# Kernel optimization log

Measured on AMD Instinct MI355X. Metric: run time of the kernel, lower is better.

## Reference

```python
import jax, jax.numpy as jnp
import numpy as np

N = 50000      # nodes
E = 800000     # edges (avg degree 16)
D = 128        # in_channels
H = 128        # hidden_channels


def sage_conv(x, edge_index, W_l, b_l, W_r):
    """PyG SAGEConv with aggr='mean': lin_l(mean_j x_j) + lin_r(x_i).
    edge_index[0] = source (j), edge_index[1] = destination (i)."""
    src, dst = edge_index[0], edge_index[1]
    n = x.shape[0]
    msg = x[src]                                               # [E, D] gather
    agg = jax.ops.segment_sum(msg, dst, num_segments=n)        # [N, D] scatter-sum
    cnt = jax.ops.segment_sum(jnp.ones((src.shape[0],), x.dtype), dst, num_segments=n)
    agg = agg / jnp.maximum(cnt, 1.0)[:, None]                 # mean (0 for isolated nodes)
    return agg @ W_l.T + b_l + x @ W_r.T


def setup_inputs() -> dict:
    key = jax.random.key(0)
    ks = jax.random.split(key, 9)
    s_in = 1.0 / np.sqrt(D)
    s_h = 1.0 / np.sqrt(H)
    return {
        "x": jax.random.normal(ks[0], (N, D), dtype=jnp.float32),
        "edge_index": jax.random.randint(ks[1], (2, E), 0, N, dtype=jnp.int64),
        "W1l": jax.random.uniform(ks[2], (H, D), jnp.float32, -s_in, s_in),
        "b1l": jnp.zeros((H,), jnp.float32),
        "W1r": jax.random.uniform(ks[3], (H, D), jnp.float32, -s_in, s_in),
        "W2l": jax.random.uniform(ks[4], (H, H), jnp.float32, -s_h, s_h),
        "b2l": jnp.zeros((H,), jnp.float32),
        "W2r": jax.random.uniform(ks[5], (H, H), jnp.float32, -s_h, s_h),
        "W3l": jax.random.uniform(ks[6], (H, H), jnp.float32, -s_h, s_h),
        "b3l": jnp.zeros((H,), jnp.float32),
        "W3r": jax.random.uniform(ks[7], (H, H), jnp.float32, -s_h, s_h),
    }


def reference(x, edge_index, W1l, b1l, W1r, W2l, b2l, W2r, W3l, b3l, W3r):
    x1 = sage_conv(x, edge_index, W1l, b1l, W1r)
    x1 = jax.nn.relu(x1)  # Dropout(0.5) treated as identity (eval mode)
    h_ = sage_conv(x1, edge_index, W2l, b2l, W2r)
    h = sage_conv(x1, edge_index, W3l, b3l, W3r)
    return (h_, h)
```

## Files before the change

kernel.cpp:

```cpp
#include <hip/hip_runtime.h>
#include <stdint.h>
#include <math.h>

typedef __attribute__((ext_vector_type(8))) short short8;
typedef __attribute__((ext_vector_type(4))) float float4v;

__device__ __forceinline__ uint16_t f2bf(float f){
  union { float f; uint32_t i; } c; c.f = f;
  uint32_t r = c.i + 0x7fffu + ((c.i >> 16) & 1u);
  return (uint16_t)(r >> 16);
}
__device__ __forceinline__ uint32_t pack2(float lo, float hi){
  return (uint32_t)f2bf(lo) | ((uint32_t)f2bf(hi) << 16);
}
__device__ __forceinline__ void acc_bf2(uint32_t w, float& x, float& y){
  union { uint32_t i; float f; } a, b;
  a.i = w << 16; b.i = w & 0xffff0000u;
  x += a.f; y += b.f;
}
__device__ __forceinline__ void accum8(uint4 v, float* a){
  acc_bf2(v.x, a[0], a[1]); acc_bf2(v.y, a[2], a[3]);
  acc_bf2(v.z, a[4], a[5]); acc_bf2(v.w, a[6], a[7]);
}


__global__ __launch_bounds__(512) void prep_kernel(
    const int* __restrict__ ei, int E, int NB, int CAP, int p1blk,
    int* __restrict__ fill, uint32_t* __restrict__ bins,
    const float* __restrict__ x,
    const float* __restrict__ w0, const float* __restrict__ w1,
    const float* __restrict__ w2, const float* __restrict__ w3,
    const float* __restrict__ w4, const float* __restrict__ w5,
    uint16_t* __restrict__ xb, uint16_t* __restrict__ wb, int nx){
  if ((int)blockIdx.x < p1blk){
    __shared__ int hist[256], scn[256], cursor[256], gbase[256], excl[256];
    __shared__ uint32_t stage[4096];
    int tid = threadIdx.x;
    if (tid < 256) hist[tid] = 0;
    __syncthreads();
    int e0 = blockIdx.x * 4096;
    int nval = E - e0; if (nval > 4096) nval = 4096;
    uint32_t w[8]; int bk[8];
    #pragma unroll
    for (int k = 0; k < 8; ++k){
      int e = e0 + k * 512 + tid;
      bool ok = e < E;
      int s = ok ? ei[e] : 0;
      int d = ok ? ei[E + e] : 0;
      w[k] = (uint32_t)s | ((uint32_t)d << 16);
      bk[k] = ok ? (d >> 8) : -1;
      if (ok) atomicAdd(&hist[bk[k]], 1);
    }
    __syncthreads();
    if (tid < 256) scn[tid] = hist[tid];
    __syncthreads();
    #pragma unroll
    for (int off = 1; off < 256; off <<= 1){
      int v = 0;
      if (tid < 256 && tid >= off) v = scn[tid - off];
      __syncthreads();
      if (tid < 256) scn[tid] += v;
      __syncthreads();
    }
    if (tid < 256){
      int ex = scn[tid] - hist[tid];
      excl[tid] = ex; cursor[tid] = ex;
      gbase[tid] = (tid < NB && hist[tid] > 0)
                   ? atomicAdd(&fill[tid], hist[tid]) : 0;
    }
    __syncthreads();
    #pragma unroll
    for (int k = 0; k < 8; ++k){
      if (bk[k] >= 0){
        int p = atomicAdd(&cursor[bk[k]], 1);
        stage[p] = w[k];
      }
    }
    __syncthreads();
    for (int i = tid; i < nval; i += 512){
      uint32_t v = stage[i];
      int b = v >> 24;
      int loc = gbase[b] + (i - excl[b]);
      if (loc < CAP)
        __builtin_nontemporal_store(v, bins + (size_t)b * CAP + loc);
    }
  } else {
    int i = (blockIdx.x - p1blk) * 512 + threadIdx.x;
    int stride = (gridDim.x - p1blk) * 512;
    for (int j = i; j < (nx >> 2); j += stride){
      float4 v = ((const float4*)x)[j];
      uint2 o;
      o.x = pack2(v.x, v.y); o.y = pack2(v.z, v.w);
      ((uint2*)xb)[j] = o;
    }
    const int WSZ = 128 * 128;
    for (int j = i; j < 6 * WSZ; j += stride){
      int t = j >> 14, o = j & (WSZ - 1);
      const float* w = t == 0 ? w0 : t == 1 ? w1 : t == 2 ? w2 : t == 3 ? w3 : t == 4 ? w4 : w5;
      wb[j] = f2bf(w[o]);
    }
  }
}


__global__ __launch_bounds__(512) void build_kernel(const uint32_t* __restrict__ bins,
                                                    const int* __restrict__ fill,
                                                    int CAP, int n,
                                                    int2* __restrict__ rowptr2,
                                                    uint32_t* __restrict__ esrc){
  __shared__ int hist[256], scn[256], cursor[256], excl[256];
  __shared__ uint32_t stage[5120];
  int b = blockIdx.x, tid = threadIdx.x;
  int cnt = fill[b]; if (cnt > CAP) cnt = CAP; if (cnt > 5120) cnt = 5120;
  size_t gb = (size_t)b * CAP;
  if (tid < 256) hist[tid] = 0;
  __syncthreads();
  for (int i = tid; i < cnt; i += 512)
    atomicAdd(&hist[(bins[gb + i] >> 16) & 255], 1);
  __syncthreads();
  if (tid < 256) scn[tid] = hist[tid];
  __syncthreads();
  #pragma unroll
  for (int off = 1; off < 256; off <<= 1){
    int v = 0;
    if (tid < 256 && tid >= off) v = scn[tid - off];
    __syncthreads();
    if (tid < 256) scn[tid] += v;
    __syncthreads();
  }
  if (tid < 256){
    int ex = scn[tid] - hist[tid];
    excl[tid] = ex; cursor[tid] = ex;
    int node = (b << 8) + tid;
    if (node < n) rowptr2[node] = make_int2((int)gb + ex, (int)gb + scn[tid]);
  }
  __syncthreads();
  for (int i = tid; i < cnt; i += 512){
    uint32_t v = bins[gb + i];
    int p = atomicAdd(&cursor[(v >> 16) & 255], 1);
    stage[p] = v & 0xffffu;
  }
  __syncthreads();
  for (int i = tid; i < cnt; i += 512)
    __builtin_nontemporal_store(stage[i], esrc + gb + i);
}


__global__ __launch_bounds__(256) void agg_kernel(const uint16_t* __restrict__ xin,
                                                  const int2* __restrict__ rowptr2,
                                                  const uint32_t* __restrict__ esrc,
                                                  uint16_t* __restrict__ aggw, int n){
  int node = blockIdx.x * 4 + (threadIdx.x >> 6);
  if (node >= n) return;
  int lane = threadIdx.x & 63;
  int sub = lane >> 4, fq = lane & 15;
  const uint4* xv = (const uint4*)xin;
  int2 be = rowptr2[node];
  int beg = be.x, end = be.y;
  float inv = 1.f / fmaxf((float)(end - beg), 1.f);
  float a[8] = {0.f,0.f,0.f,0.f,0.f,0.f,0.f,0.f};
  int e = beg + sub;
  for (; e + 12 < end; e += 16){
    int s0 = esrc[e], s1 = esrc[e + 4], s2 = esrc[e + 8], s3 = esrc[e + 12];
    uint4 v0 = xv[(size_t)s0 * 16 + fq];
    uint4 v1 = xv[(size_t)s1 * 16 + fq];
    uint4 v2 = xv[(size_t)s2 * 16 + fq];
    uint4 v3 = xv[(size_t)s3 * 16 + fq];
    accum8(v0, a); accum8(v1, a); accum8(v2, a); accum8(v3, a);
  }
  for (; e < end; e += 4){
    uint4 v = xv[(size_t)esrc[e] * 16 + fq];
    accum8(v, a);
  }
  #pragma unroll
  for (int i = 0; i < 8; ++i){
    a[i] += __shfl_xor(a[i], 16);
    a[i] += __shfl_xor(a[i], 32);
    a[i] *= inv;
  }
  if (sub == 0){
    uint4 o;
    o.x = pack2(a[0], a[1]); o.y = pack2(a[2], a[3]);
    o.z = pack2(a[4], a[5]); o.w = pack2(a[6], a[7]);
    ((uint4*)aggw)[(size_t)node * 16 + fq] = o;
  }
}


#define WT_STRIDE 136

__device__ __forceinline__ void stage_weights(const uint16_t* __restrict__ Wl,
                                              const uint16_t* __restrict__ Wr,
                                              int ch, uint16_t* lds_l,
                                              uint16_t* lds_r, int tid){
  const uint4* srcL = (const uint4*)(Wl + (size_t)(ch * 64) * 128);
  const uint4* srcR = (const uint4*)(Wr + (size_t)(ch * 64) * 128);
  #pragma unroll
  for (int i = 0; i < 4; ++i){
    int j = tid + i * 256;
    int row = j >> 4, c8 = j & 15;
    uint4 vl = srcL[j], vr = srcR[j];
    *(uint4*)(lds_l + row * WT_STRIDE + c8 * 8) = vl;
    *(uint4*)(lds_r + row * WT_STRIDE + c8 * 8) = vr;
  }
}

__global__ __launch_bounds__(256) void gemm1_kernel(
    const uint16_t* __restrict__ Aagg, const uint16_t* __restrict__ Ax,
    const uint16_t* __restrict__ Wl, const uint16_t* __restrict__ Wr,
    const float* __restrict__ bias, uint16_t* __restrict__ x1b, int n){
  __shared__ uint16_t lds_l[64 * WT_STRIDE], lds_r[64 * WT_STRIDE];
  int tid = threadIdx.x, lane = tid & 63, wid = tid >> 6;
  int m = lane & 15, quad = lane >> 4;
  int r0 = blockIdx.x * 64 + wid * 16;
  int arow = r0 + m; if (arow > n - 1) arow = n - 1;

  short8 a0f[4], a1f[4];
  #pragma unroll
  for (int ks = 0; ks < 4; ++ks){
    a0f[ks] = *(const short8*)(Aagg + (size_t)arow * 128 + ks * 32 + quad * 8);
    a1f[ks] = *(const short8*)(Ax   + (size_t)arow * 128 + ks * 32 + quad * 8);
  }

  for (int ch = 0; ch < 2; ++ch){
    if (ch) __syncthreads();
    stage_weights(Wl, Wr, ch, lds_l, lds_r, tid);
    __syncthreads();
    float4v acc[4];
    #pragma unroll
    for (int ct = 0; ct < 4; ++ct) acc[ct] = (float4v){0.f, 0.f, 0.f, 0.f};
    #pragma unroll
    for (int ks = 0; ks < 4; ++ks){
      #pragma unroll
      for (int ct = 0; ct < 4; ++ct){
        short8 b0 = *(const short8*)(lds_l + (ct * 16 + m) * WT_STRIDE + ks * 32 + quad * 8);
        acc[ct] = __builtin_amdgcn_mfma_f32_16x16x32_bf16(a0f[ks], b0, acc[ct], 0, 0, 0);
        short8 b1 = *(const short8*)(lds_r + (ct * 16 + m) * WT_STRIDE + ks * 32 + quad * 8);
        acc[ct] = __builtin_amdgcn_mfma_f32_16x16x32_bf16(a1f[ks], b1, acc[ct], 0, 0, 0);
      }
    }
    #pragma unroll
    for (int ct = 0; ct < 4; ++ct){
      int col = ch * 64 + ct * 16 + m;
      float bv = bias[col];
      #pragma unroll
      for (int i = 0; i < 4; ++i){
        int grow = r0 + quad * 4 + i;
        if (grow < n)
          x1b[(size_t)grow * 128 + col] = f2bf(fmaxf(acc[ct][i] + bv, 0.f));
      }
    }
  }
}

__global__ __launch_bounds__(256) void gemm23_kernel(
    const uint16_t* __restrict__ Aagg, const uint16_t* __restrict__ Ax,
    const uint16_t* __restrict__ W2l, const uint16_t* __restrict__ W2r,
    const float* __restrict__ b2,
    const uint16_t* __restrict__ W3l, const uint16_t* __restrict__ W3r,
    const float* __restrict__ b3,
    float* __restrict__ out, size_t half, int n){
  __shared__ uint16_t lds_l[64 * WT_STRIDE], lds_r[64 * WT_STRIDE];
  int tid = threadIdx.x, lane = tid & 63, wid = tid >> 6;
  int m = lane & 15, quad = lane >> 4;
  int r0 = blockIdx.x * 64 + wid * 16;
  int arow = r0 + m; if (arow > n - 1) arow = n - 1;

  short8 a0f[4], a1f[4];
  #pragma unroll
  for (int ks = 0; ks < 4; ++ks){
    a0f[ks] = *(const short8*)(Aagg + (size_t)arow * 128 + ks * 32 + quad * 8);
    a1f[ks] = *(const short8*)(Ax   + (size_t)arow * 128 + ks * 32 + quad * 8);
  }

  for (int idx = 0; idx < 4; ++idx){
    int pass = idx >> 1, ch = idx & 1;
    if (idx) __syncthreads();
    stage_weights(pass ? W3l : W2l, pass ? W3r : W2r, ch, lds_l, lds_r, tid);
    __syncthreads();
    float4v acc[4];
    #pragma unroll
    for (int ct = 0; ct < 4; ++ct) acc[ct] = (float4v){0.f, 0.f, 0.f, 0.f};
    #pragma unroll
    for (int ks = 0; ks < 4; ++ks){
      #pragma unroll
      for (int ct = 0; ct < 4; ++ct){
        short8 b0 = *(const short8*)(lds_l + (ct * 16 + m) * WT_STRIDE + ks * 32 + quad * 8);
        acc[ct] = __builtin_amdgcn_mfma_f32_16x16x32_bf16(a0f[ks], b0, acc[ct], 0, 0, 0);
        short8 b1 = *(const short8*)(lds_r + (ct * 16 + m) * WT_STRIDE + ks * 32 + quad * 8);
        acc[ct] = __builtin_amdgcn_mfma_f32_16x16x32_bf16(a1f[ks], b1, acc[ct], 0, 0, 0);
      }
    }
    const float* bb = pass ? b3 : b2;
    float* op = out + (pass ? half : 0);
    #pragma unroll
    for (int ct = 0; ct < 4; ++ct){
      int col = ch * 64 + ct * 16 + m;
      float bv = bb[col];
      #pragma unroll
      for (int i = 0; i < 4; ++i){
        int grow = r0 + quad * 4 + i;
        if (grow < n)
          __builtin_nontemporal_store(acc[ct][i] + bv,
                                      op + (size_t)grow * 128 + col);
      }
    }
  }
}


extern "C" void kernel_launch(void* const* d_in, const int* in_sizes, int n_in,
                              void* d_out, int out_size, void* d_ws, size_t ws_size,
                              hipStream_t stream) {
  const float* x   = (const float*)d_in[0];
  const int*   ei  = (const int*)d_in[1];
  const float* W1l = (const float*)d_in[2];
  const float* b1l = (const float*)d_in[3];
  const float* W1r = (const float*)d_in[4];
  const float* W2l = (const float*)d_in[5];
  const float* b2l = (const float*)d_in[6];
  const float* W2r = (const float*)d_in[7];
  const float* W3l = (const float*)d_in[8];
  const float* b3l = (const float*)d_in[9];
  const float* W3r = (const float*)d_in[10];
  float* out = (float*)d_out;

  const int n = in_sizes[0] / 128;
  const int E = in_sizes[1] / 2;
  const size_t half = (size_t)n * 128;
  const int WSZ = 128 * 128;

  const int NB = (n + 255) >> 8;
  int mean = (E + NB - 1) / NB;
  int CAP = mean + 8 * (int)sqrt((double)mean) + 64;
  CAP = (CAP + 63) & ~63;
  if (CAP > 5120) CAP = 5120;

  size_t off = 0;
  auto carve = [&](size_t bytes) -> void* {
    void* p = (char*)d_ws + off;
    off += (bytes + 255) & ~(size_t)255;
    return p;
  };
  int2*     rowptr2 = (int2*)carve((size_t)n * 8);
  int*      fill    = (int*)carve((size_t)NB * 4);
  uint32_t* esrc    = (uint32_t*)carve((size_t)NB * CAP * 4);
  uint16_t* xb      = (uint16_t*)carve(half * 2);
  uint16_t* wb      = (uint16_t*)carve((size_t)6 * WSZ * 2);
  uint16_t* x1b     = (uint16_t*)carve(half * 2);
  uint16_t* agg     = (uint16_t*)carve(half * 2);
  uint32_t* bins    = (uint32_t*)carve((size_t)NB * CAP * 4);
  (void)ws_size;

  hipMemsetAsync(fill, 0, (size_t)NB * 4, stream);

  int p1blk = (E + 4095) / 4096;
  int cblk  = 512;
  prep_kernel<<<p1blk + cblk, 512, 0, stream>>>(ei, E, NB, CAP, p1blk, fill, bins,
                                                x, W1l, W1r, W2l, W2r, W3l, W3r,
                                                xb, wb, (int)half);
  build_kernel<<<NB, 512, 0, stream>>>(bins, fill, CAP, n, rowptr2, esrc);

  int ablk = (n + 3) / 4;
  int gblk = (n + 63) / 64;
  const uint16_t *Wb1l = wb, *Wb1r = wb + WSZ, *Wb2l = wb + 2 * WSZ,
                 *Wb2r = wb + 3 * WSZ, *Wb3l = wb + 4 * WSZ, *Wb3r = wb + 5 * WSZ;

  agg_kernel<<<ablk, 256, 0, stream>>>(xb, rowptr2, esrc, agg, n);
  gemm1_kernel<<<gblk, 256, 0, stream>>>(agg, xb, Wb1l, Wb1r, b1l, x1b, n);

  agg_kernel<<<ablk, 256, 0, stream>>>(x1b, rowptr2, esrc, agg, n);
  gemm23_kernel<<<gblk, 256, 0, stream>>>(agg, x1b, Wb2l, Wb2r, b2l,
                                          Wb3l, Wb3r, b3l, out, half, n);
}
```

Baseline: 215.6 us.

## Split CSR build into quarter-bin blocks and parallelize gemm23 over passes

The edge binning pass now handles 2048 edges per block instead of 4096, and more blocks go to the conversion work. The CSR build kernel is split four ways per bin: each block redoes the bin histogram but only scatters the 64 nodes in its quarter, which raises parallelism and shrinks shared-memory staging. The layer-2/3 GEMM kernel gets a second grid dimension so each pass (W2 vs W3) runs in its own block. The cost is redundant histogram work and rereading each bin four times, plus the A fragments being loaded twice across the pass blocks.

```diff
diff --git a/kernel.cpp b/kernel.cpp
--- a/kernel.cpp
+++ b/kernel.cpp
@@ -23,6 +23,8 @@
   acc_bf2(v.z, a[4], a[5]); acc_bf2(v.w, a[6], a[7]);
 }
 
+
+#define P1_EPT 4
 
 __global__ __launch_bounds__(512) void prep_kernel(
     const int* __restrict__ ei, int E, int NB, int CAP, int p1blk,
@@ -34,15 +36,15 @@
     uint16_t* __restrict__ xb, uint16_t* __restrict__ wb, int nx){
   if ((int)blockIdx.x < p1blk){
     __shared__ int hist[256], scn[256], cursor[256], gbase[256], excl[256];
-    __shared__ uint32_t stage[4096];
+    __shared__ uint32_t stage[2048];
     int tid = threadIdx.x;
     if (tid < 256) hist[tid] = 0;
     __syncthreads();
-    int e0 = blockIdx.x * 4096;
-    int nval = E - e0; if (nval > 4096) nval = 4096;
-    uint32_t w[8]; int bk[8];
-    #pragma unroll
-    for (int k = 0; k < 8; ++k){
+    int e0 = blockIdx.x * 2048;
+    int nval = E - e0; if (nval > 2048) nval = 2048;
+    uint32_t w[P1_EPT]; int bk[P1_EPT];
+    #pragma unroll
+    for (int k = 0; k < P1_EPT; ++k){
       int e = e0 + k * 512 + tid;
       bool ok = e < E;
       int s = ok ? ei[e] : 0;
@@ -70,7 +72,7 @@
     }
     __syncthreads();
     #pragma unroll
-    for (int k = 0; k < 8; ++k){
+    for (int k = 0; k < P1_EPT; ++k){
       if (bk[k] >= 0){
         int p = atomicAdd(&cursor[bk[k]], 1);
         stage[p] = w[k];
@@ -108,10 +110,11 @@
                                                     int CAP, int n,
                                                     int2* __restrict__ rowptr2,
                                                     uint32_t* __restrict__ esrc){
-  __shared__ int hist[256], scn[256], cursor[256], excl[256];
-  __shared__ uint32_t stage[5120];
-  int b = blockIdx.x, tid = threadIdx.x;
-  int cnt = fill[b]; if (cnt > CAP) cnt = CAP; if (cnt > 5120) cnt = 5120;
+  __shared__ int hist[256], scn[256], cursor[64];
+  __shared__ uint32_t stage[4096];
+  int blk = blockIdx.x, tid = threadIdx.x;
+  int b = blk >> 2, q = blk & 3;
+  int cnt = fill[b]; if (cnt > CAP) cnt = CAP;
   size_t gb = (size_t)b * CAP;
   if (tid < 256) hist[tid] = 0;
   __syncthreads();
@@ -128,21 +131,30 @@
     if (tid < 256) scn[tid] += v;
     __syncthreads();
   }
-  if (tid < 256){
-    int ex = scn[tid] - hist[tid];
-    excl[tid] = ex; cursor[tid] = ex;
-    int node = (b << 8) + tid;
-    if (node < n) rowptr2[node] = make_int2((int)gb + ex, (int)gb + scn[tid]);
+  int q0 = q * 64;
+  int qstart = scn[q0] - hist[q0];
+  int qend = scn[q0 + 63];
+  if (tid < 64){
+    int idx = q0 + tid;
+    int node = (b << 8) + idx;
+    int ex = scn[idx] - hist[idx];
+    cursor[tid] = ex - qstart;
+    if (node < n) rowptr2[node] = make_int2((int)gb + ex, (int)gb + scn[idx]);
   }
   __syncthreads();
   for (int i = tid; i < cnt; i += 512){
     uint32_t v = bins[gb + i];
-    int p = atomicAdd(&cursor[(v >> 16) & 255], 1);
-    stage[p] = v & 0xffffu;
-  }
-  __syncthreads();
-  for (int i = tid; i < cnt; i += 512)
-    __builtin_nontemporal_store(stage[i], esrc + gb + i);
+    int nb = (v >> 16) & 255;
+    int r = nb - q0;
+    if ((unsigned)r < 64u){
+      int p = atomicAdd(&cursor[r], 1);
+      if (p < 4096) stage[p] = v & 0xffffu;
+    }
+  }
+  __syncthreads();
+  int qcnt = qend - qstart; if (qcnt > 4096) qcnt = 4096;
+  for (int i = tid; i < qcnt; i += 512)
+    __builtin_nontemporal_store(stage[i], esrc + gb + qstart + i);
 }
 
 
@@ -263,6 +275,11 @@
   __shared__ uint16_t lds_l[64 * WT_STRIDE], lds_r[64 * WT_STRIDE];
   int tid = threadIdx.x, lane = tid & 63, wid = tid >> 6;
   int m = lane & 15, quad = lane >> 4;
+  int pass = blockIdx.y;
+  const uint16_t* Wl = pass ? W3l : W2l;
+  const uint16_t* Wr = pass ? W3r : W2r;
+  const float*    bb = pass ? b3  : b2;
+  float* op = out + (pass ? half : 0);
   int r0 = blockIdx.x * 64 + wid * 16;
   int arow = r0 + m; if (arow > n - 1) arow = n - 1;
 
@@ -273,10 +290,9 @@
     a1f[ks] = *(const short8*)(Ax   + (size_t)arow * 128 + ks * 32 + quad * 8);
   }
 
-  for (int idx = 0; idx < 4; ++idx){
-    int pass = idx >> 1, ch = idx & 1;
-    if (idx) __syncthreads();
-    stage_weights(pass ? W3l : W2l, pass ? W3r : W2r, ch, lds_l, lds_r, tid);
+  for (int ch = 0; ch < 2; ++ch){
+    if (ch) __syncthreads();
+    stage_weights(Wl, Wr, ch, lds_l, lds_r, tid);
     __syncthreads();
     float4v acc[4];
     #pragma unroll
@@ -291,8 +307,6 @@
         acc[ct] = __builtin_amdgcn_mfma_f32_16x16x32_bf16(a1f[ks], b1, acc[ct], 0, 0, 0);
       }
     }
-    const float* bb = pass ? b3 : b2;
-    float* op = out + (pass ? half : 0);
     #pragma unroll
     for (int ct = 0; ct < 4; ++ct){
       int col = ch * 64 + ct * 16 + m;
@@ -354,12 +368,12 @@
 
   hipMemsetAsync(fill, 0, (size_t)NB * 4, stream);
 
-  int p1blk = (E + 4095) / 4096;
-  int cblk  = 512;
+  int p1blk = (E + 2047) / 2048;
+  int cblk  = 768;
   prep_kernel<<<p1blk + cblk, 512, 0, stream>>>(ei, E, NB, CAP, p1blk, fill, bins,
                                                 x, W1l, W1r, W2l, W2r, W3l, W3r,
                                                 xb, wb, (int)half);
-  build_kernel<<<NB, 512, 0, stream>>>(bins, fill, CAP, n, rowptr2, esrc);
+  build_kernel<<<NB * 4, 512, 0, stream>>>(bins, fill, CAP, n, rowptr2, esrc);
 
   int ablk = (n + 3) / 4;
   int gblk = (n + 63) / 64;
@@ -370,6 +384,6 @@
   gemm1_kernel<<<gblk, 256, 0, stream>>>(agg, xb, Wb1l, Wb1r, b1l, x1b, n);
 
   agg_kernel<<<ablk, 256, 0, stream>>>(x1b, rowptr2, esrc, agg, n);
-  gemm23_kernel<<<gblk, 256, 0, stream>>>(agg, x1b, Wb2l, Wb2r, b2l,
-                                          Wb3l, Wb3r, b3l, out, half, n);
-}
+  gemm23_kernel<<<dim3(gblk, 2), 256, 0, stream>>>(agg, x1b, Wb2l, Wb2r, b2l,
+                                                   Wb3l, Wb3r, b3l, out, half, n);
+}
```

New measurement: 222.6 us. 3.3% more time.

## Fuse all pipeline stages into one cooperative persistent kernel with grid syncs

Applied to the files above, without the earlier changes.

Replaces the six separate kernel launches (prep, build, two agg, two gemm) with a single cooperative mega-kernel that uses grid-wide syncs between phases and grid-stride loops over work. The aim is to remove launch overhead and inter-kernel gaps. In exchange, occupancy is bounded by the persistent grid size, and grid.sync barriers add cost. The old multi-kernel path is kept as a fallback if the cooperative launch fails. It also drops a 5120 clamp in build_kernel that guarded the stage buffer.

```diff
diff --git a/kernel.cpp b/kernel.cpp
--- a/kernel.cpp
+++ b/kernel.cpp
@@ -1,6 +1,9 @@
 #include <hip/hip_runtime.h>
+#include <hip/hip_cooperative_groups.h>
 #include <stdint.h>
 #include <math.h>
+
+namespace cg = cooperative_groups;
 
 typedef __attribute__((ext_vector_type(8))) short short8;
 typedef __attribute__((ext_vector_type(4))) float float4v;
@@ -21,6 +24,308 @@
 __device__ __forceinline__ void accum8(uint4 v, float* a){
   acc_bf2(v.x, a[0], a[1]); acc_bf2(v.y, a[2], a[3]);
   acc_bf2(v.z, a[4], a[5]); acc_bf2(v.w, a[6], a[7]);
+}
+
+#define WT_STRIDE 136
+
+
+struct MegaParams {
+  const int* ei;
+  const float *x, *W1l, *b1l, *W1r, *W2l, *b2l, *W2r, *W3l, *b3l, *W3r;
+  float* out;
+  int* fill; uint32_t* bins; uint32_t* esrc; int2* rowptr2;
+  uint16_t *xb, *wb, *x1b, *agg;
+  int E, n, NB, CAP, p1blk;
+  size_t half;
+};
+
+__device__ __forceinline__ void agg_phase(const uint16_t* __restrict__ xin,
+                                          const int2* __restrict__ rowptr2,
+                                          const uint32_t* __restrict__ esrc,
+                                          uint16_t* __restrict__ aggw,
+                                          int n, int tid, int bid, int gsz){
+  int wid = tid >> 6, lane = tid & 63;
+  int sub = lane >> 4, fq = lane & 15;
+  const uint4* xv = (const uint4*)xin;
+  for (int node = bid * 8 + wid; node < n; node += gsz * 8){
+    int2 be = rowptr2[node];
+    int beg = be.x, end = be.y;
+    float inv = 1.f / fmaxf((float)(end - beg), 1.f);
+    float a[8] = {0.f,0.f,0.f,0.f,0.f,0.f,0.f,0.f};
+    int e = beg + sub;
+    for (; e + 12 < end; e += 16){
+      int s0 = esrc[e], s1 = esrc[e + 4], s2 = esrc[e + 8], s3 = esrc[e + 12];
+      uint4 v0 = xv[(size_t)s0 * 16 + fq];
+      uint4 v1 = xv[(size_t)s1 * 16 + fq];
+      uint4 v2 = xv[(size_t)s2 * 16 + fq];
+      uint4 v3 = xv[(size_t)s3 * 16 + fq];
+      accum8(v0, a); accum8(v1, a); accum8(v2, a); accum8(v3, a);
+    }
+    for (; e < end; e += 4){
+      uint4 v = xv[(size_t)esrc[e] * 16 + fq];
+      accum8(v, a);
+    }
+    #pragma unroll
+    for (int i = 0; i < 8; ++i){
+      a[i] += __shfl_xor(a[i], 16);
+      a[i] += __shfl_xor(a[i], 32);
+      a[i] *= inv;
+    }
+    if (sub == 0){
+      uint4 o;
+      o.x = pack2(a[0], a[1]); o.y = pack2(a[2], a[3]);
+      o.z = pack2(a[4], a[5]); o.w = pack2(a[6], a[7]);
+      ((uint4*)aggw)[(size_t)node * 16 + fq] = o;
+    }
+  }
+}
+
+__device__ __forceinline__ void stage_weights512(const uint16_t* __restrict__ Wl,
+                                                 const uint16_t* __restrict__ Wr,
+                                                 int ch, uint16_t* lds_l,
+                                                 uint16_t* lds_r, int tid){
+  const uint4* srcL = (const uint4*)(Wl + (size_t)(ch * 64) * 128);
+  const uint4* srcR = (const uint4*)(Wr + (size_t)(ch * 64) * 128);
+  #pragma unroll
+  for (int i = 0; i < 2; ++i){
+    int j = tid + i * 512;
+    int row = j >> 4, c8 = j & 15;
+    uint4 vl = srcL[j], vr = srcR[j];
+    *(uint4*)(lds_l + row * WT_STRIDE + c8 * 8) = vl;
+    *(uint4*)(lds_r + row * WT_STRIDE + c8 * 8) = vr;
+  }
+}
+
+__global__ __launch_bounds__(512, 6) void mega_kernel(MegaParams P){
+  cg::grid_group gg = cg::this_grid();
+  __shared__ __align__(16) uint8_t smem[34816];
+  const int tid = threadIdx.x, bid = blockIdx.x, gsz = gridDim.x;
+  const int WSZ = 128 * 128;
+
+  if (bid < P.p1blk){
+    int* hist = (int*)smem;
+    int* scn  = hist + 256;
+    int* cur  = hist + 512;
+    int* gbas = hist + 768;
+    int* excl = hist + 1024;
+    uint32_t* stg = (uint32_t*)(smem + 5120);
+    if (tid < 256) hist[tid] = 0;
+    __syncthreads();
+    int e0 = bid * 4096;
+    int nval = P.E - e0; if (nval > 4096) nval = 4096;
+    uint32_t w[8]; int bk[8];
+    #pragma unroll
+    for (int k = 0; k < 8; ++k){
+      int e = e0 + k * 512 + tid;
+      bool ok = e < P.E;
+      int s = ok ? P.ei[e] : 0;
+      int d = ok ? P.ei[P.E + e] : 0;
+      w[k] = (uint32_t)s | ((uint32_t)d << 16);
+      bk[k] = ok ? (d >> 8) : -1;
+      if (ok) atomicAdd(&hist[bk[k]], 1);
+    }
+    __syncthreads();
+    if (tid < 256) scn[tid] = hist[tid];
+    __syncthreads();
+    #pragma unroll
+    for (int off = 1; off < 256; off <<= 1){
+      int v = 0;
+      if (tid < 256 && tid >= off) v = scn[tid - off];
+      __syncthreads();
+      if (tid < 256) scn[tid] += v;
+      __syncthreads();
+    }
+    if (tid < 256){
+      int ex = scn[tid] - hist[tid];
+      excl[tid] = ex; cur[tid] = ex;
+      gbas[tid] = (tid < P.NB && hist[tid] > 0)
+                  ? atomicAdd(&P.fill[tid], hist[tid]) : 0;
+    }
+    __syncthreads();
+    #pragma unroll
+    for (int k = 0; k < 8; ++k){
+      if (bk[k] >= 0){
+        int p = atomicAdd(&cur[bk[k]], 1);
+        stg[p] = w[k];
+      }
+    }
+    __syncthreads();
+    for (int i = tid; i < nval; i += 512){
+      uint32_t v = stg[i];
+      int b = v >> 24;
+      int loc = gbas[b] + (i - excl[b]);
+      if (loc < P.CAP)
+        __builtin_nontemporal_store(v, P.bins + (size_t)b * P.CAP + loc);
+    }
+  } else {
+    int i0 = (bid - P.p1blk) * 512 + tid;
+    int stride = (gsz - P.p1blk) * 512;
+    int nx4 = (P.n * 128) >> 2;
+    for (int j = i0; j < nx4; j += stride){
+      float4 v = ((const float4*)P.x)[j];
+      uint2 o; o.x = pack2(v.x, v.y); o.y = pack2(v.z, v.w);
+      ((uint2*)P.xb)[j] = o;
+    }
+    for (int j = i0; j < 6 * WSZ; j += stride){
+      int t = j >> 14, o = j & (WSZ - 1);
+      const float* w = t == 0 ? P.W1l : t == 1 ? P.W1r : t == 2 ? P.W2l
+                     : t == 3 ? P.W2r : t == 4 ? P.W3l : P.W3r;
+      P.wb[j] = f2bf(w[o]);
+    }
+  }
+  gg.sync();
+
+  for (int b = bid; b < P.NB; b += gsz){
+    int* hist = (int*)smem; int* scn = hist + 256; int* cursor = hist + 512;
+    uint32_t* stage = (uint32_t*)(smem + 3072);
+    int cnt = P.fill[b]; if (cnt > P.CAP) cnt = P.CAP;
+    size_t gb = (size_t)b * P.CAP;
+    if (tid < 256) hist[tid] = 0;
+    __syncthreads();
+    for (int i = tid; i < cnt; i += 512)
+      atomicAdd(&hist[(P.bins[gb + i] >> 16) & 255], 1);
+    __syncthreads();
+    if (tid < 256) scn[tid] = hist[tid];
+    __syncthreads();
+    #pragma unroll
+    for (int off = 1; off < 256; off <<= 1){
+      int v = 0;
+      if (tid < 256 && tid >= off) v = scn[tid - off];
+      __syncthreads();
+      if (tid < 256) scn[tid] += v;
+      __syncthreads();
+    }
+    if (tid < 256){
+      int ex = scn[tid] - hist[tid];
+      cursor[tid] = ex;
+      int node = (b << 8) + tid;
+      if (node < P.n) P.rowptr2[node] = make_int2((int)gb + ex, (int)gb + scn[tid]);
+    }
+    __syncthreads();
+    for (int i = tid; i < cnt; i += 512){
+      uint32_t v = P.bins[gb + i];
+      int p = atomicAdd(&cursor[(v >> 16) & 255], 1);
+      stage[p] = v & 0xffffu;
+    }
+    __syncthreads();
+    for (int i = tid; i < cnt; i += 512)
+      __builtin_nontemporal_store(stage[i], P.esrc + gb + i);
+    __syncthreads();
+  }
+  gg.sync();
+
+  agg_phase(P.xb, P.rowptr2, P.esrc, P.agg, P.n, tid, bid, gsz);
+  gg.sync();
+
+  {
+    uint16_t* lds_l = (uint16_t*)smem;
+    uint16_t* lds_r = lds_l + 64 * WT_STRIDE;
+    int lane = tid & 63, wid = tid >> 6;
+    int m = lane & 15, quad = lane >> 4;
+    const uint16_t* Wl = P.wb;
+    const uint16_t* Wr = P.wb + WSZ;
+    int ngt = (P.n + 63) >> 6;
+    int nt2 = (ngt + 1) >> 1;
+    for (int t2 = bid; t2 < nt2; t2 += gsz){
+      int tile = t2 * 2 + (wid >> 2);
+      int r0 = tile * 64 + (wid & 3) * 16;
+      int arow = r0 + m; if (arow > P.n - 1) arow = P.n - 1;
+      short8 a0f[4], a1f[4];
+      #pragma unroll
+      for (int ks = 0; ks < 4; ++ks){
+        a0f[ks] = *(const short8*)(P.agg + (size_t)arow * 128 + ks * 32 + quad * 8);
+        a1f[ks] = *(const short8*)(P.xb  + (size_t)arow * 128 + ks * 32 + quad * 8);
+      }
+      for (int ch = 0; ch < 2; ++ch){
+        __syncthreads();
+        stage_weights512(Wl, Wr, ch, lds_l, lds_r, tid);
+        __syncthreads();
+        float4v acc[4];
+        #pragma unroll
+        for (int ct = 0; ct < 4; ++ct) acc[ct] = (float4v){0.f, 0.f, 0.f, 0.f};
+        #pragma unroll
+        for (int ks = 0; ks < 4; ++ks){
+          #pragma unroll
+          for (int ct = 0; ct < 4; ++ct){
+            short8 b0 = *(const short8*)(lds_l + (ct * 16 + m) * WT_STRIDE + ks * 32 + quad * 8);
+            acc[ct] = __builtin_amdgcn_mfma_f32_16x16x32_bf16(a0f[ks], b0, acc[ct], 0, 0, 0);
+            short8 b1 = *(const short8*)(lds_r + (ct * 16 + m) * WT_STRIDE + ks * 32 + quad * 8);
+            acc[ct] = __builtin_amdgcn_mfma_f32_16x16x32_bf16(a1f[ks], b1, acc[ct], 0, 0, 0);
+          }
+        }
+        #pragma unroll
+        for (int ct = 0; ct < 4; ++ct){
+          int col = ch * 64 + ct * 16 + m;
+          float bv = P.b1l[col];
+          #pragma unroll
+          for (int i = 0; i < 4; ++i){
+            int grow = r0 + quad * 4 + i;
+            if (grow < P.n)
+              P.x1b[(size_t)grow * 128 + col] = f2bf(fmaxf(acc[ct][i] + bv, 0.f));
+          }
+        }
+      }
+    }
+  }
+  gg.sync();
+
+  agg_phase(P.x1b, P.rowptr2, P.esrc, P.agg, P.n, tid, bid, gsz);
+  gg.sync();
+
+  {
+    uint16_t* lds_l = (uint16_t*)smem;
+    uint16_t* lds_r = lds_l + 64 * WT_STRIDE;
+    int lane = tid & 63, wid = tid >> 6;
+    int m = lane & 15, quad = lane >> 4;
+    int ngt = (P.n + 63) >> 6;
+    int nt2 = (ngt + 1) >> 1;
+    for (int t2 = bid; t2 < nt2; t2 += gsz){
+      int tile = t2 * 2 + (wid >> 2);
+      int r0 = tile * 64 + (wid & 3) * 16;
+      int arow = r0 + m; if (arow > P.n - 1) arow = P.n - 1;
+      short8 a0f[4], a1f[4];
+      #pragma unroll
+      for (int ks = 0; ks < 4; ++ks){
+        a0f[ks] = *(const short8*)(P.agg + (size_t)arow * 128 + ks * 32 + quad * 8);
+        a1f[ks] = *(const short8*)(P.x1b + (size_t)arow * 128 + ks * 32 + quad * 8);
+      }
+      for (int idx = 0; idx < 4; ++idx){
+        int pass = idx >> 1, ch = idx & 1;
+        const uint16_t* Wl = P.wb + (pass ? 4 : 2) * WSZ;
+        const uint16_t* Wr = P.wb + (pass ? 5 : 3) * WSZ;
+        __syncthreads();
+        stage_weights512(Wl, Wr, ch, lds_l, lds_r, tid);
+        __syncthreads();
+        float4v acc[4];
+        #pragma unroll
+        for (int ct = 0; ct < 4; ++ct) acc[ct] = (float4v){0.f, 0.f, 0.f, 0.f};
+        #pragma unroll
+        for (int ks = 0; ks < 4; ++ks){
+          #pragma unroll
+          for (int ct = 0; ct < 4; ++ct){
+            short8 b0 = *(const short8*)(lds_l + (ct * 16 + m) * WT_STRIDE + ks * 32 + quad * 8);
+            acc[ct] = __builtin_amdgcn_mfma_f32_16x16x32_bf16(a0f[ks], b0, acc[ct], 0, 0, 0);
+            short8 b1 = *(const short8*)(lds_r + (ct * 16 + m) * WT_STRIDE + ks * 32 + quad * 8);
+            acc[ct] = __builtin_amdgcn_mfma_f32_16x16x32_bf16(a1f[ks], b1, acc[ct], 0, 0, 0);
+          }
+        }
+        const float* bb = pass ? P.b3l : P.b2l;
+        float* op = P.out + (pass ? P.half : 0);
+        #pragma unroll
+        for (int ct = 0; ct < 4; ++ct){
+          int col = ch * 64 + ct * 16 + m;
+          float bv = bb[col];
+          #pragma unroll
+          for (int i = 0; i < 4; ++i){
+            int grow = r0 + quad * 4 + i;
+            if (grow < P.n)
+              __builtin_nontemporal_store(acc[ct][i] + bv,
+                                          op + (size_t)grow * 128 + col);
+          }
+        }
+      }
+    }
+  }
 }
 
 
@@ -102,16 +407,15 @@
   }
 }
 
-
 __global__ __launch_bounds__(512) void build_kernel(const uint32_t* __restrict__ bins,
                                                     const int* __restrict__ fill,
                                                     int CAP, int n,
                                                     int2* __restrict__ rowptr2,
                                                     uint32_t* __restrict__ esrc){
-  __shared__ int hist[256], scn[256], cursor[256], excl[256];
+  __shared__ int hist[256], scn[256], cursor[256];
   __shared__ uint32_t stage[5120];
   int b = blockIdx.x, tid = threadIdx.x;
-  int cnt = fill[b]; if (cnt > CAP) cnt = CAP; if (cnt > 5120) cnt = 5120;
+  int cnt = fill[b]; if (cnt > CAP) cnt = CAP;
   size_t gb = (size_t)b * CAP;
   if (tid < 256) hist[tid] = 0;
   __syncthreads();
@@ -130,7 +434,7 @@
   }
   if (tid < 256){
     int ex = scn[tid] - hist[tid];
-    excl[tid] = ex; cursor[tid] = ex;
+    cursor[tid] = ex;
     int node = (b << 8) + tid;
     if (node < n) rowptr2[node] = make_int2((int)gb + ex, (int)gb + scn[tid]);
   }
@@ -144,7 +448,6 @@
   for (int i = tid; i < cnt; i += 512)
     __builtin_nontemporal_store(stage[i], esrc + gb + i);
 }
-
 
 __global__ __launch_bounds__(256) void agg_kernel(const uint16_t* __restrict__ xin,
                                                   const int2* __restrict__ rowptr2,
@@ -186,9 +489,6 @@
   }
 }
 
-
-#define WT_STRIDE 136
-
 __device__ __forceinline__ void stage_weights(const uint16_t* __restrict__ Wl,
                                               const uint16_t* __restrict__ Wr,
                                               int ch, uint16_t* lds_l,
@@ -214,14 +514,12 @@
   int m = lane & 15, quad = lane >> 4;
   int r0 = blockIdx.x * 64 + wid * 16;
   int arow = r0 + m; if (arow > n - 1) arow = n - 1;
-
   short8 a0f[4], a1f[4];
   #pragma unroll
   for (int ks = 0; ks < 4; ++ks){
     a0f[ks] = *(const short8*)(Aagg + (size_t)arow * 128 + ks * 32 + quad * 8);
     a1f[ks] = *(const short8*)(Ax   + (size_t)arow * 128 + ks * 32 + quad * 8);
   }
-
   for (int ch = 0; ch < 2; ++ch){
     if (ch) __syncthreads();
     stage_weights(Wl, Wr, ch, lds_l, lds_r, tid);
@@ -265,14 +563,12 @@
   int m = lane & 15, quad = lane >> 4;
   int r0 = blockIdx.x * 64 + wid * 16;
   int arow = r0 + m; if (arow > n - 1) arow = n - 1;
-
   short8 a0f[4], a1f[4];
   #pragma unroll
   for (int ks = 0; ks < 4; ++ks){
     a0f[ks] = *(const short8*)(Aagg + (size_t)arow * 128 + ks * 32 + quad * 8);
     a1f[ks] = *(const short8*)(Ax   + (size_t)arow * 128 + ks * 32 + quad * 8);
   }
-
   for (int idx = 0; idx < 4; ++idx){
     int pass = idx >> 1, ch = idx & 1;
     if (idx) __syncthreads();
@@ -355,7 +651,36 @@
   hipMemsetAsync(fill, 0, (size_t)NB * 4, stream);
 
   int p1blk = (E + 4095) / 4096;
-  int cblk  = 512;
+
+  static int grid = 0;
+  if (grid == 0){
+    int perCU = 0;
+    if (hipOccupancyMaxActiveBlocksPerMultiprocessor(&perCU,
+            (const void*)mega_kernel, 512, 0) != hipSuccess || perCU < 1)
+      perCU = 1;
+    grid = perCU * 256;
+    if (grid > 1024) grid = 1024;
+    if (grid < 256)  grid = 256;
+  }
+
+  MegaParams mp;
+  mp.ei = ei; mp.x = x;
+  mp.W1l = W1l; mp.b1l = b1l; mp.W1r = W1r;
+  mp.W2l = W2l; mp.b2l = b2l; mp.W2r = W2r;
+  mp.W3l = W3l; mp.b3l = b3l; mp.W3r = W3r;
+  mp.out = out;
+  mp.fill = fill; mp.bins = bins; mp.esrc = esrc; mp.rowptr2 = rowptr2;
+  mp.xb = xb; mp.wb = wb; mp.x1b = x1b; mp.agg = agg;
+  mp.E = E; mp.n = n; mp.NB = NB; mp.CAP = CAP; mp.p1blk = p1blk;
+  mp.half = half;
+
+  void* args[] = { &mp };
+  hipError_t err = hipLaunchCooperativeKernel((const void*)mega_kernel,
+                                              dim3(grid), dim3(512),
+                                              args, 0, stream);
+  if (err == hipSuccess) return;
+
+  int cblk = 512;
   prep_kernel<<<p1blk + cblk, 512, 0, stream>>>(ei, E, NB, CAP, p1blk, fill, bins,
                                                 x, W1l, W1r, W2l, W2r, W3l, W3r,
                                                 xb, wb, (int)half);
@@ -368,7 +693,6 @@
 
   agg_kernel<<<ablk, 256, 0, stream>>>(xb, rowptr2, esrc, agg, n);
   gemm1_kernel<<<gblk, 256, 0, stream>>>(agg, xb, Wb1l, Wb1r, b1l, x1b, n);
-
   agg_kernel<<<ablk, 256, 0, stream>>>(x1b, rowptr2, esrc, agg, n);
   gemm23_kernel<<<gblk, 256, 0, stream>>>(agg, x1b, Wb2l, Wb2r, b2l,
                                           Wb3l, Wb3r, b3l, out, half, n);
```

Result: slower. 486.0 us (+125.4%).
